# Performance work log

Measured on AMD Instinct MI355X. Metric: run time of the kernel, lower is better.

The kernel has to match this reference:

```python
import jax, jax.numpy as jnp
import numpy as np

LOWER = 300  # hidden size of the critic MLP


def setup_inputs() -> dict:
    key = jax.random.key(0)
    ks = jax.random.split(key, 6)
    N, XD, YD = 1024, 768, 768
    x = jax.random.normal(ks[0], (N, XD), dtype=jnp.float32)
    y = jax.random.normal(ks[1], (N, YD), dtype=jnp.float32)
    # Linear(x_dim+y_dim -> LOWER), Linear(LOWER -> 1); Kaiming-uniform-ish init
    b1_lim = 1.0 / np.sqrt(XD + YD)
    b2_lim = 1.0 / np.sqrt(LOWER)
    W1 = jax.random.uniform(ks[2], (XD + YD, LOWER), jnp.float32, -b1_lim, b1_lim)
    b1 = jax.random.uniform(ks[3], (LOWER,), jnp.float32, -b1_lim, b1_lim)
    W2 = jax.random.uniform(ks[4], (LOWER, 1), jnp.float32, -b2_lim, b2_lim)
    b2 = jax.random.uniform(ks[5], (1,), jnp.float32, -b2_lim, b2_lim)
    return {"x_samples": x, "y_samples": y, "W1": W1, "b1": b1, "W2": W2, "b2": b2}


def reference(x_samples, y_samples, W1, b1, W2, b2):
    N = y_samples.shape[0]
    xd = x_samples.shape[-1]
    # Decompose first Linear: cat([x, y]) @ W1 == x @ W1[:xd] + y @ W1[xd:]
    Wx, Wy = W1[:xd], W1[xd:]
    hx = x_samples @ Wx          # [N, LOWER]
    hy = y_samples @ Wy          # [N, LOWER]
    w2 = W2[:, 0]                # [LOWER]

    def critic(h):
        # relu -> Linear(LOWER->1) -> softplus
        return jax.nn.softplus(jax.nn.relu(h) @ w2 + b2[0])

    # T0[i] = F(x[i], y[i])
    T0 = critic(hx + hy + b1)                       # [N]
    # T1[i, j] = F(x[j], y[i])  (x tiled over dim 0, y over dim 1)
    h_pair = hy[:, None, :] + hx[None, :, :] + b1   # [N, N, LOWER]
    T1 = critic(h_pair)                             # [N, N]
    lower_bound = (T0.mean()
                   - jax.nn.logsumexp(T1, axis=1).mean()
                   - jnp.log(jnp.float32(N)))
    return lower_bound
```

## Files before the change

kernel.cpp:

```cpp
#include <hip/hip_runtime.h>
#include <math.h>

#define N_S 1024
#define XD  768
#define LOW 300
#define KP  320
#define KP2 160

typedef _Float16 h2  __attribute__((ext_vector_type(2)));
typedef __fp16   g2  __attribute__((ext_vector_type(2)));
typedef _Float16 v8h __attribute__((ext_vector_type(8)));
typedef float    f4  __attribute__((ext_vector_type(4)));

union U32H2 { unsigned int u; h2 h; };
__device__ inline h2 u2h(unsigned int v){ U32H2 t; t.u = v; return t.h; }
__device__ inline unsigned int pk(float a, float b){
    g2 t = __builtin_amdgcn_cvt_pkrtz(a, b);
    return __builtin_bit_cast(unsigned int, t);
}
union U4V8 { uint4 u; v8h v; };

__global__ __launch_bounds__(512)
void gemm_h(const float* __restrict__ x, const float* __restrict__ y,
            const float* __restrict__ W1, const float* __restrict__ b1g,
            unsigned int* __restrict__ hx_h, unsigned int* __restrict__ hy_h,
            float* __restrict__ partsum, unsigned int* __restrict__ cnt)
{
    __shared__ unsigned int As[2][32][36];
    __shared__ unsigned int Bs[2][64][36];

    const int tid = threadIdx.x;
    const int job = blockIdx.x;
    if (job < 256 && tid < 4) partsum[job * 4 + tid] = 0.f;
    if (job == 0 && tid == 4) cnt[0] = 0u;

    const int which = job >= 160;
    const int t = which ? job - 160 : job;
    const int n0 = (t % 5) * 64;
    const int r0 = (t / 5) * 32;
    const float* A = which ? y : x;
    const float* W = W1 + (size_t)which * XD * LOW;
    _Float16* outh = (_Float16*)(which ? hy_h : hx_h);

    const int w = tid >> 6, l = tid & 63;
    const int wm = w >> 2, wn = w & 3;
    const int lr = l & 15, lg = l >> 4;

    const int arow = tid >> 4, aq = tid & 15;
    const int bn = tid & 63, bms = tid >> 6;
    const bool bin = (n0 + bn) < LOW;

    f4 acc = {};
    float4 a0; float bw[8];
    a0 = *(const float4*)&A[(size_t)(r0 + arow) * XD + aq * 4];
    #pragma unroll
    for (int s = 0; s < 8; ++s)
        bw[s] = bin ? W[(size_t)(bms * 8 + s) * LOW + n0 + bn] : 0.f;

    const int NC = XD / 64;
    for (int c = 0; c < NC; ++c) {
        const int buf = c & 1;
        *(uint2*)&As[buf][arow][aq * 2] = make_uint2(pk(a0.x, a0.y), pk(a0.z, a0.w));
        *(uint4*)&Bs[buf][bn][bms * 4] =
            uint4{ pk(bw[0],bw[1]), pk(bw[2],bw[3]), pk(bw[4],bw[5]), pk(bw[6],bw[7]) };
        __syncthreads();
        if (c + 1 < NC) {
            const int kb = (c + 1) * 64;
            a0 = *(const float4*)&A[(size_t)(r0 + arow) * XD + kb + aq * 4];
            #pragma unroll
            for (int s = 0; s < 8; ++s)
                bw[s] = bin ? W[(size_t)(kb + bms * 8 + s) * LOW + n0 + bn] : 0.f;
        }
        #pragma unroll
        for (int ks = 0; ks < 2; ++ks) {
            const int ko = ks * 16 + lg * 4;
            U4V8 af; af.u = *(const uint4*)&As[buf][wm * 16 + lr][ko];
            U4V8 bf; bf.u = *(const uint4*)&Bs[buf][wn * 16 + lr][ko];
            acc = __builtin_amdgcn_mfma_f32_16x16x32_f16(af.v, bf.v, acc, 0, 0, 0);
        }
    }

    const int col = n0 + wn * 16 + lr;
    const float b1v = (which && col < LOW) ? b1g[col] : 0.f;
    #pragma unroll
    for (int r = 0; r < 4; ++r) {
        const int row = r0 + wm * 16 + lg * 4 + r;
        outh[(size_t)row * KP + col] = (_Float16)(acc[r] + b1v);
    }
}

__global__ __launch_bounds__(256)
void pair_kernel(const unsigned int* __restrict__ hx_h, const unsigned int* __restrict__ hy_h,
                 const float* __restrict__ W2, const float* __restrict__ b2,
                 float* __restrict__ partsum, float* __restrict__ diag,
                 unsigned int* __restrict__ cnt, float* __restrict__ out)
{
    const int b0 = blockIdx.x;
    const int bs = (b0 & 7) * 64 + (b0 >> 3);
    const int jb = bs & 15, ib = bs >> 4;
    const int j0 = jb * 64, i0 = ib * 32;

    __shared__ unsigned int Hy[32][160];
    __shared__ unsigned int Hx[64][160];
    __shared__ unsigned int w2s[KP2];
    __shared__ unsigned int lastFlag;
    __shared__ float ssum[4];

    const int tid = threadIdx.x;

    {
        const int r = tid >> 3, sq = tid & 7;
        const unsigned int* sy = &hy_h[(size_t)(i0 + r) * KP2];
        #pragma unroll
        for (int e = 0; e < 5; ++e) {
            const int s = sq + 8 * e;
            *(uint4*)&Hy[r][s * 4] = *(const uint4*)&sy[s * 4];
        }
    }
    {
        #pragma unroll
        for (int rp = 0; rp < 2; ++rp) {
            const int r = (tid >> 3) + 32 * rp, sq = tid & 7;
            const unsigned int* sx = &hx_h[(size_t)(j0 + r) * KP2];
            const int swz = (r >> 2) & 7;
            #pragma unroll
            for (int e = 0; e < 5; ++e) {
                const int s = sq + 8 * e;
                *(uint4*)&Hx[r][(s ^ swz) * 4] = *(const uint4*)&sx[s * 4];
            }
        }
    }
    if (tid < KP2) {
        int k = tid * 2;
        float w0 = (k < LOW) ? W2[k] : 0.f;
        float w1 = (k + 1 < LOW) ? W2[k + 1] : 0.f;
        w2s[tid] = pk(w0, w1);
    }
    __syncthreads();

    const int tx = tid & 15;
    const int kh = (tid >> 4) & 1;
    const int iy = tid >> 5;
    const int xsw = tx & 7;

    float accf[4][4] = {};
    const h2 hz = h2{(_Float16)0.f, (_Float16)0.f};
    const int tb = kh * 20;

    for (int tc = 0; tc < 5; ++tc) {
        h2 acch[4][4];
        #pragma unroll
        for (int r = 0; r < 4; ++r)
            #pragma unroll
            for (int q = 0; q < 4; ++q) acch[r][q] = hz;

        #pragma unroll
        for (int ti = 0; ti < 4; ++ti) {
            const int t = tb + tc * 4 + ti;
            uint4 ya[4], xb[4];
            #pragma unroll
            for (int r = 0; r < 4; ++r)
                ya[r] = *(const uint4*)&Hy[iy * 4 + r][t * 4];
            const int sx = (t ^ xsw) * 4;
            #pragma unroll
            for (int q = 0; q < 4; ++q)
                xb[q] = *(const uint4*)&Hx[tx * 4 + q][sx];
            const uint4 wv = *(const uint4*)&w2s[t * 4];
            const unsigned int wve[4] = {wv.x, wv.y, wv.z, wv.w};
            #pragma unroll
            for (int e = 0; e < 4; ++e) {
                const h2 w = u2h(wve[e]);
                const unsigned int yae[4] = {ya[0][e], ya[1][e], ya[2][e], ya[3][e]};
                const unsigned int xbe[4] = {xb[0][e], xb[1][e], xb[2][e], xb[3][e]};
                #pragma unroll
                for (int r = 0; r < 4; ++r) {
                    const h2 a = u2h(yae[r]);
                    #pragma unroll
                    for (int q = 0; q < 4; ++q) {
                        h2 z = __builtin_elementwise_max(a + u2h(xbe[q]), hz);
                        acch[r][q] = __builtin_elementwise_fma(z, w, acch[r][q]);
                    }
                }
            }
        }
        #pragma unroll
        for (int r = 0; r < 4; ++r)
            #pragma unroll
            for (int q = 0; q < 4; ++q)
                accf[r][q] += (float)acch[r][q][0] + (float)acch[r][q][1];
    }

    #pragma unroll
    for (int r = 0; r < 4; ++r)
        #pragma unroll
        for (int q = 0; q < 4; ++q)
            accf[r][q] += __shfl_xor(accf[r][q], 16, 64);

    const float b2v = b2[0];
    #pragma unroll
    for (int r = 0; r < 4; ++r) {
        const int row = i0 + iy * 4 + r;
        float es = 0.f;
        #pragma unroll
        for (int q = 0; q < 4; ++q) {
            const float s = accf[r][q] + b2v;
            es += __expf(s);
            const int col = j0 + tx * 4 + q;
            if (col == row)
                atomicExch(&diag[row],
                           fmaxf(s, 0.f) + __logf(1.f + __expf(-fabsf(s))));
        }
        #pragma unroll
        for (int o = 1; o <= 8; o <<= 1) es += __shfl_xor(es, o, 64);
        if ((tid & 31) == 0) atomicAdd(&partsum[row], es);
    }

    asm volatile("s_waitcnt vmcnt(0)" ::: "memory");
    __syncthreads();
    if (tid == 0) lastFlag = (atomicAdd(cnt, 1u) == 511u) ? 1u : 0u;
    __syncthreads();
    if (!lastFlag) return;

    float csum = 0.f;
    #pragma unroll
    for (int g = 0; g < 4; ++g) {
        const int row = g * 256 + tid;
        const float ps = atomicAdd(&partsum[row], 0.f);
        const float dg = atomicAdd(&diag[row], 0.f);
        csum += dg - __logf((float)N_S + ps);
    }
    #pragma unroll
    for (int o = 32; o > 0; o >>= 1) csum += __shfl_xor(csum, o, 64);
    if ((tid & 63) == 0) ssum[tid >> 6] = csum;
    __syncthreads();
    if (tid == 0)
        out[0] = (ssum[0] + ssum[1] + ssum[2] + ssum[3]) * (1.0f / N_S)
               - logf((float)N_S);
}

extern "C" void kernel_launch(void* const* d_in, const int* in_sizes, int n_in,
                              void* d_out, int out_size, void* d_ws, size_t ws_size,
                              hipStream_t stream)
{
    const float* x  = (const float*)d_in[0];
    const float* y  = (const float*)d_in[1];
    const float* W1 = (const float*)d_in[2];
    const float* b1 = (const float*)d_in[3];
    const float* W2 = (const float*)d_in[4];
    const float* b2 = (const float*)d_in[5];
    float* outp = (float*)d_out;

    unsigned int* hx_h = (unsigned int*)d_ws;
    unsigned int* hy_h = hx_h + (size_t)N_S * KP2;
    float* partsum = (float*)(hy_h + (size_t)N_S * KP2);
    float* diag = partsum + N_S;
    unsigned int* cnt = (unsigned int*)(diag + N_S);

    gemm_h<<<320, 512, 0, stream>>>(x, y, W1, b1, hx_h, hy_h, partsum, cnt);

    pair_kernel<<<512, 256, 0, stream>>>(hx_h, hy_h, W2, b2,
                                         partsum, diag, cnt, outp);
}
```

Baseline: 43.84 us.

## Use fdot2 f32 accumulation and split K over four groups with 512 threads

```diff
diff --git a/kernel.cpp b/kernel.cpp
--- a/kernel.cpp
+++ b/kernel.cpp
@@ -89,7 +89,7 @@
     }
 }
 
-__global__ __launch_bounds__(256)
+__global__ __launch_bounds__(512)
 void pair_kernel(const unsigned int* __restrict__ hx_h, const unsigned int* __restrict__ hy_h,
                  const float* __restrict__ W2, const float* __restrict__ b2,
                  float* __restrict__ partsum, float* __restrict__ diag,
@@ -100,34 +100,31 @@
     const int jb = bs & 15, ib = bs >> 4;
     const int j0 = jb * 64, i0 = ib * 32;
 
-    __shared__ unsigned int Hy[32][160];
-    __shared__ unsigned int Hx[64][160];
+    __shared__ unsigned int Hy[32][164];
+    __shared__ unsigned int Hx[64][164];
     __shared__ unsigned int w2s[KP2];
     __shared__ unsigned int lastFlag;
-    __shared__ float ssum[4];
+    __shared__ float ssum[8];
 
     const int tid = threadIdx.x;
 
+    {
+        const int r = tid >> 4, sq = tid & 15;
+        const unsigned int* sy = &hy_h[(size_t)(i0 + r) * KP2];
+        #pragma unroll
+        for (int e = 0; e < 3; ++e) {
+            const int s = sq + 16 * e;
+            if (s < 40)
+                *(uint4*)&Hy[r][s * 4] = *(const uint4*)&sy[s * 4];
+        }
+    }
     {
         const int r = tid >> 3, sq = tid & 7;
-        const unsigned int* sy = &hy_h[(size_t)(i0 + r) * KP2];
+        const unsigned int* sx = &hx_h[(size_t)(j0 + r) * KP2];
         #pragma unroll
         for (int e = 0; e < 5; ++e) {
             const int s = sq + 8 * e;
-            *(uint4*)&Hy[r][s * 4] = *(const uint4*)&sy[s * 4];
-        }
-    }
-    {
-        #pragma unroll
-        for (int rp = 0; rp < 2; ++rp) {
-            const int r = (tid >> 3) + 32 * rp, sq = tid & 7;
-            const unsigned int* sx = &hx_h[(size_t)(j0 + r) * KP2];
-            const int swz = (r >> 2) & 7;
-            #pragma unroll
-            for (int e = 0; e < 5; ++e) {
-                const int s = sq + 8 * e;
-                *(uint4*)&Hx[r][(s ^ swz) * 4] = *(const uint4*)&sx[s * 4];
-            }
+            *(uint4*)&Hx[r][s * 4] = *(const uint4*)&sx[s * 4];
         }
     }
     if (tid < KP2) {
@@ -139,62 +136,51 @@
     __syncthreads();
 
     const int tx = tid & 15;
-    const int kh = (tid >> 4) & 1;
-    const int iy = tid >> 5;
-    const int xsw = tx & 7;
-
-    float accf[4][4] = {};
+    const int kh = (tid >> 4) & 3;
+    const int iy = tid >> 6;
+
+    float acc[4][4] = {};
     const h2 hz = h2{(_Float16)0.f, (_Float16)0.f};
-    const int tb = kh * 20;
-
-    for (int tc = 0; tc < 5; ++tc) {
-        h2 acch[4][4];
+    const int tb = kh * 10;
+
+    #pragma unroll 2
+    for (int ti = 0; ti < 10; ++ti) {
+        const int t = tb + ti;
+        uint4 ya[4], xb[4];
         #pragma unroll
         for (int r = 0; r < 4; ++r)
+            ya[r] = *(const uint4*)&Hy[iy * 4 + r][t * 4];
+        #pragma unroll
+        for (int q = 0; q < 4; ++q)
+            xb[q] = *(const uint4*)&Hx[tx * 4 + q][t * 4];
+        const uint4 wv = *(const uint4*)&w2s[t * 4];
+        const unsigned int wve[4] = {wv.x, wv.y, wv.z, wv.w};
+        #pragma unroll
+        for (int e = 0; e < 4; ++e) {
+            const h2 w = u2h(wve[e]);
+            const unsigned int yae[4] = {ya[0][e], ya[1][e], ya[2][e], ya[3][e]};
+            const unsigned int xbe[4] = {xb[0][e], xb[1][e], xb[2][e], xb[3][e]};
             #pragma unroll
-            for (int q = 0; q < 4; ++q) acch[r][q] = hz;
-
-        #pragma unroll
-        for (int ti = 0; ti < 4; ++ti) {
-            const int t = tb + tc * 4 + ti;
-            uint4 ya[4], xb[4];
-            #pragma unroll
-            for (int r = 0; r < 4; ++r)
-                ya[r] = *(const uint4*)&Hy[iy * 4 + r][t * 4];
-            const int sx = (t ^ xsw) * 4;
-            #pragma unroll
-            for (int q = 0; q < 4; ++q)
-                xb[q] = *(const uint4*)&Hx[tx * 4 + q][sx];
-            const uint4 wv = *(const uint4*)&w2s[t * 4];
-            const unsigned int wve[4] = {wv.x, wv.y, wv.z, wv.w};
-            #pragma unroll
-            for (int e = 0; e < 4; ++e) {
-                const h2 w = u2h(wve[e]);
-                const unsigned int yae[4] = {ya[0][e], ya[1][e], ya[2][e], ya[3][e]};
-                const unsigned int xbe[4] = {xb[0][e], xb[1][e], xb[2][e], xb[3][e]};
+            for (int r = 0; r < 4; ++r) {
+                const h2 a = u2h(yae[r]);
                 #pragma unroll
-                for (int r = 0; r < 4; ++r) {
-                    const h2 a = u2h(yae[r]);
-                    #pragma unroll
-                    for (int q = 0; q < 4; ++q) {
-                        h2 z = __builtin_elementwise_max(a + u2h(xbe[q]), hz);
-                        acch[r][q] = __builtin_elementwise_fma(z, w, acch[r][q]);
-                    }
+                for (int q = 0; q < 4; ++q) {
+                    h2 z = __builtin_elementwise_max(a + u2h(xbe[q]), hz);
+                    acc[r][q] = __builtin_amdgcn_fdot2(z, w, acc[r][q], false);
                 }
             }
         }
-        #pragma unroll
-        for (int r = 0; r < 4; ++r)
-            #pragma unroll
-            for (int q = 0; q < 4; ++q)
-                accf[r][q] += (float)acch[r][q][0] + (float)acch[r][q][1];
     }
 
     #pragma unroll
     for (int r = 0; r < 4; ++r)
         #pragma unroll
-        for (int q = 0; q < 4; ++q)
-            accf[r][q] += __shfl_xor(accf[r][q], 16, 64);
+        for (int q = 0; q < 4; ++q) {
+            float v = acc[r][q];
+            v += __shfl_xor(v, 16, 64);
+            v += __shfl_xor(v, 32, 64);
+            acc[r][q] = v;
+        }
 
     const float b2v = b2[0];
     #pragma unroll
@@ -203,7 +189,7 @@
         float es = 0.f;
         #pragma unroll
         for (int q = 0; q < 4; ++q) {
-            const float s = accf[r][q] + b2v;
+            const float s = acc[r][q] + b2v;
             es += __expf(s);
             const int col = j0 + tx * 4 + q;
             if (col == row)
@@ -212,7 +198,7 @@
         }
         #pragma unroll
         for (int o = 1; o <= 8; o <<= 1) es += __shfl_xor(es, o, 64);
-        if ((tid & 31) == 0) atomicAdd(&partsum[row], es);
+        if ((tid & 63) == 0) atomicAdd(&partsum[row], es);
     }
 
     asm volatile("s_waitcnt vmcnt(0)" ::: "memory");
@@ -223,8 +209,8 @@
 
     float csum = 0.f;
     #pragma unroll
-    for (int g = 0; g < 4; ++g) {
-        const int row = g * 256 + tid;
+    for (int g = 0; g < 2; ++g) {
+        const int row = g * 512 + tid;
         const float ps = atomicAdd(&partsum[row], 0.f);
         const float dg = atomicAdd(&diag[row], 0.f);
         csum += dg - __logf((float)N_S + ps);
@@ -233,9 +219,12 @@
     for (int o = 32; o > 0; o >>= 1) csum += __shfl_xor(csum, o, 64);
     if ((tid & 63) == 0) ssum[tid >> 6] = csum;
     __syncthreads();
-    if (tid == 0)
-        out[0] = (ssum[0] + ssum[1] + ssum[2] + ssum[3]) * (1.0f / N_S)
-               - logf((float)N_S);
+    if (tid == 0) {
+        float t = 0.f;
+        #pragma unroll
+        for (int q = 0; q < 8; ++q) t += ssum[q];
+        out[0] = t * (1.0f / N_S) - logf((float)N_S);
+    }
 }
 
 extern "C" void kernel_launch(void* const* d_in, const int* in_sizes, int n_in,
@@ -258,6 +247,6 @@
 
     gemm_h<<<320, 512, 0, stream>>>(x, y, W1, b1, hx_h, hy_h, partsum, cnt);
 
-    pair_kernel<<<512, 256, 0, stream>>>(hx_h, hy_h, W2, b2,
+    pair_kernel<<<512, 512, 0, stream>>>(hx_h, hy_h, W2, b2,
                                          partsum, diag, cnt, outp);
 }
```

Measured after the change: 43.17 us. No clear change (-1.5%).
